# Optimization experiments

Hardware: AMD Instinct MI355X
Metric: run time of the kernel (lower is better)

The kernel has to match this reference:

```python
import jax, jax.numpy as jnp
import numpy as np

N_HEAD = 16
LN_EPS = 1e-5


def _ln(x, w, b):
    # torch LayerNorm computed in float32 then cast back (see LayerNorm.forward)
    xf = x.astype(jnp.float32)
    mu = jnp.mean(xf, axis=-1, keepdims=True)
    var = jnp.mean(jnp.square(xf - mu), axis=-1, keepdims=True)
    return ((xf - mu) * jax.lax.rsqrt(var + LN_EPS) * w + b).astype(x.dtype)


def setup_inputs() -> dict:
    key = jax.random.key(0)
    ks = jax.random.split(key, 16)
    B, S, C = 4, 1500, 1024
    A = 256  # adapter_dim
    F = 4 * C
    s = 0.02
    return {
        "x": jax.random.normal(ks[0], (B, S, C), jnp.float32),
        "Wq": jax.random.normal(ks[1], (C, C), jnp.float32) * s,
        "bq": jnp.zeros((C,), jnp.float32),
        "Wk": jax.random.normal(ks[2], (C, C), jnp.float32) * s,
        "Wv": jax.random.normal(ks[3], (C, C), jnp.float32) * s,
        "bv": jnp.zeros((C,), jnp.float32),
        "Wo": jax.random.normal(ks[4], (C, C), jnp.float32) * s,
        "bo": jnp.zeros((C,), jnp.float32),
        "ln_attn_w": jnp.ones((C,), jnp.float32),
        "ln_attn_b": jnp.zeros((C,), jnp.float32),
        "W1": jax.random.normal(ks[5], (F, C), jnp.float32) * s,
        "b1": jnp.zeros((F,), jnp.float32),
        "W2": jax.random.normal(ks[6], (C, F), jnp.float32) * s,
        "b2": jnp.zeros((C,), jnp.float32),
        "ln_mlp_w": jnp.ones((C,), jnp.float32),
        "ln_mlp_b": jnp.zeros((C,), jnp.float32),
        "Wds": jax.random.normal(ks[7], (A, C), jnp.float32) * s,
        "bds": jnp.zeros((A,), jnp.float32),
        "Wus": jax.random.normal(ks[8], (C, A), jnp.float32) * s,
        "bus": jnp.zeros((C,), jnp.float32),
    }


def reference(x, Wq, bq, Wk, Wv, bv, Wo, bo, ln_attn_w, ln_attn_b,
              W1, b1, W2, b2, ln_mlp_w, ln_mlp_b, Wds, bds, Wus, bus):
    B, S, C = x.shape
    H = N_HEAD
    D = C // H
    scale = D ** -0.25  # applied to both q and k, per qkv_attention

    # --- self-attention ---
    h = _ln(x, ln_attn_w, ln_attn_b)
    q = (h @ Wq.T + bq).reshape(B, S, H, D) * scale
    k = (h @ Wk.T).reshape(B, S, H, D) * scale  # key has no bias
    v = (h @ Wv.T + bv).reshape(B, S, H, D)
    qk = jnp.einsum("bqhd,bkhd->bhqk", q, k).astype(jnp.float32)
    w = jax.nn.softmax(qk, axis=-1).astype(x.dtype)
    wv = jnp.einsum("bhqk,bkhd->bqhd", w, v).reshape(B, S, C)
    x = x + (wv @ Wo.T + bo)

    # --- MLP (exact GELU, as nn.GELU default) ---
    h = _ln(x, ln_mlp_w, ln_mlp_b)
    x = x + (jax.nn.gelu(h @ W1.T + b1, approximate=False) @ W2.T + b2)

    # --- bottleneck adapter: x + us(gelu(ds(x))) ---
    x = x + (jax.nn.gelu(x @ Wds.T + bds, approximate=False) @ Wus.T + bus)
    return x
```

## Files before the change

### kernel.cpp

```cpp
#include <hip/hip_runtime.h>
#include <hip/hip_bf16.h>
#include <math.h>

typedef __bf16 bf16;
typedef __bf16 bf16x8 __attribute__((ext_vector_type(8)));
typedef float  f32x4  __attribute__((ext_vector_type(4)));

__device__ __forceinline__ void load16_lds(const bf16* g, bf16* l) {
    __builtin_amdgcn_global_load_lds(
        (__attribute__((address_space(1))) void*)(g),
        (__attribute__((address_space(3))) void*)(l), 16, 0, 0);
}

__device__ __forceinline__ float gelu_f(float x) {
    float u = 1.5957691216057308f * (x + 0.044715f * x * x * x);
    float e = __expf(u);
    float th = 1.0f - 2.0f / (1.0f + e);
    return 0.5f * x * (1.0f + th);
}

struct ConvArgs {
    const float* src[19];
    bf16* dst[19];
    int n[19];
    int bstart[20];
};
__global__ __launch_bounds__(256) void convert_many(ConvArgs a) {
    int blk = blockIdx.x;
    int s = 0;
    while (blk >= a.bstart[s + 1]) s++;
    const float* src = a.src[s];
    bf16* dst = a.dst[s];
    int n = a.n[s];
    int i0 = (blk - a.bstart[s]) * 2048;
#pragma unroll
    for (int e = 0; e < 8; e++) {
        int i = i0 + threadIdx.x + e * 256;
        if (i < n) dst[i] = (bf16)src[i];
    }
}

__global__ void zero_kernel(bf16* dst, int n) {
    int i = blockIdx.x * blockDim.x + threadIdx.x;
    if (i < n) dst[i] = (bf16)0.0f;
}

template<int ACT, int RES, class RT, class OT>
__global__ __launch_bounds__(256) void reduce_kernel(
    const bf16* __restrict__ P0, const bf16* __restrict__ P1,
    const bf16* __restrict__ bias, const RT* __restrict__ resid,
    OT* __restrict__ out, int nmask, int total)
{
    int i = (blockIdx.x * 256 + threadIdx.x) * 8;
    if (i >= total) return;
    bf16x8 p0 = *(const bf16x8*)(P0 + i);
    bf16x8 p1 = *(const bf16x8*)(P1 + i);
    bf16x8 bb = *(const bf16x8*)(bias + (i & nmask));
#pragma unroll
    for (int j = 0; j < 8; j++) {
        float v = (float)p0[j] + (float)p1[j] + (float)bb[j];
        if (ACT) v = gelu_f(v);
        if (RES) v += (float)resid[i + j];
        out[i + j] = (OT)v;
    }
}

template<class XT>
__global__ __launch_bounds__(256) void ln_kernel(
    const XT* __restrict__ X, const bf16* __restrict__ w,
    const bf16* __restrict__ b, bf16* __restrict__ out)
{
    const int C = 1024;
    const int row = blockIdx.x;
    const int tid = threadIdx.x;
    const XT* xr = X + (size_t)row * C;
    float x0 = (float)xr[tid * 4 + 0], x1 = (float)xr[tid * 4 + 1];
    float x2 = (float)xr[tid * 4 + 2], x3 = (float)xr[tid * 4 + 3];
    float s  = x0 + x1 + x2 + x3;
    float sq = x0*x0 + x1*x1 + x2*x2 + x3*x3;
#pragma unroll
    for (int off = 32; off >= 1; off >>= 1) {
        s  += __shfl_xor(s,  off, 64);
        sq += __shfl_xor(sq, off, 64);
    }
    __shared__ float red[8];
    int wave = tid >> 6;
    if ((tid & 63) == 0) { red[wave] = s; red[4 + wave] = sq; }
    __syncthreads();
    float ts = red[0] + red[1] + red[2] + red[3];
    float tq = red[4] + red[5] + red[6] + red[7];
    float mean = ts * (1.0f / C);
    float var  = tq * (1.0f / C) - mean * mean;
    float rstd = rsqrtf(var + 1e-5f);
    float w0 = (float)w[tid*4+0], w1 = (float)w[tid*4+1], w2 = (float)w[tid*4+2], w3 = (float)w[tid*4+3];
    float b0 = (float)b[tid*4+0], b1 = (float)b[tid*4+1], b2 = (float)b[tid*4+2], b3 = (float)b[tid*4+3];
    bf16* orow = out + (size_t)row * C + tid * 4;
    orow[0] = (bf16)((x0 - mean) * rstd * w0 + b0);
    orow[1] = (bf16)((x1 - mean) * rstd * w1 + b1);
    orow[2] = (bf16)((x2 - mean) * rstd * w2 + b2);
    orow[3] = (bf16)((x3 - mean) * rstd * w3 + b3);
}

template<int ACT, int OMODE, int BK2, class RT, class OT>
__global__ __launch_bounds__(256) void gemm_kernel(
    const bf16* __restrict__ A, const bf16* __restrict__ W,
    const bf16* __restrict__ bias, const RT* __restrict__ resid,
    OT* __restrict__ out, bf16* __restrict__ out_k, bf16* __restrict__ out_v,
    int M, int N, int K, float scale, int gmT, int gnT, int mQ, int ldK)
{
    const int lin = blockIdx.x;
    const int xcd = lin & 7;
    const int t_  = lin >> 3;
    const int mt_ = (xcd & 3) + 4 * (t_ % mQ);
    const int nt_ = (xcd >> 2) + 2 * (t_ / mQ);
    if (mt_ >= gmT || nt_ >= gnT) return;
    const int m0 = mt_ * 128;
    const int n0 = nt_ * 128;
    const int ksp = (OMODE == 3) ? blockIdx.y : 0;
    const size_t ko = (size_t)ksp * K;

    __shared__ __align__(16) bf16 As[8 * BK2 * 512];
    __shared__ __align__(16) bf16 Bs[8 * BK2 * 512];
    const int tid = threadIdx.x;
    const int wave = tid >> 6, lane = tid & 63;
    const int lane15 = lane & 15, quad = lane >> 4;
    const int wm0 = (wave >> 1) * 64;
    const int wn0 = (wave & 1) * 64;
    f32x4 acc[4][4] = {};

    int ra0 = m0 + (2 * wave)     * 16 + lane15; if (ra0 > M - 1) ra0 = M - 1;
    int ra1 = m0 + (2 * wave + 1) * 16 + lane15; if (ra1 > M - 1) ra1 = M - 1;
    const int rb0 = n0 + (2 * wave)     * 16 + lane15;
    const int rb1 = n0 + (2 * wave + 1) * 16 + lane15;
    const bf16* a0 = A + (size_t)ra0 * ldK + ko + quad * 8;
    const bf16* a1 = A + (size_t)ra1 * ldK + ko + quad * 8;
    const bf16* w0 = W + (size_t)rb0 * ldK + ko + quad * 8;
    const bf16* w1 = W + (size_t)rb1 * ldK + ko + quad * 8;

    for (int k0 = 0; k0 < K; k0 += 32 * BK2) {
#pragma unroll
        for (int kk = 0; kk < BK2; kk++) {
            load16_lds(a0 + k0 + kk * 32, &As[((2 * wave)     * BK2 + kk) * 512]);
            load16_lds(a1 + k0 + kk * 32, &As[((2 * wave + 1) * BK2 + kk) * 512]);
            load16_lds(w0 + k0 + kk * 32, &Bs[((2 * wave)     * BK2 + kk) * 512]);
            load16_lds(w1 + k0 + kk * 32, &Bs[((2 * wave + 1) * BK2 + kk) * 512]);
        }
        __syncthreads();
#pragma unroll
        for (int kk = 0; kk < BK2; kk++) {
            bf16x8 af[4], bfr[4];
#pragma unroll
            for (int tt = 0; tt < 4; tt++) {
                af[tt]  = *(const bf16x8*)(&As[(((wm0 >> 4) + tt) * BK2 + kk) * 512 + lane * 8]);
                bfr[tt] = *(const bf16x8*)(&Bs[(((wn0 >> 4) + tt) * BK2 + kk) * 512 + lane * 8]);
            }
#pragma unroll
            for (int mt = 0; mt < 4; mt++)
#pragma unroll
                for (int nt = 0; nt < 4; nt++)
                    acc[mt][nt] = __builtin_amdgcn_mfma_f32_16x16x32_bf16(
                        af[mt], bfr[nt], acc[mt][nt], 0, 0, 0);
        }
        __syncthreads();
    }

#pragma unroll
    for (int mt = 0; mt < 4; mt++) {
#pragma unroll
        for (int r = 0; r < 4; r++) {
            int gm = m0 + wm0 + mt * 16 + quad * 4 + r;
            if (gm >= M) continue;
#pragma unroll
            for (int nt = 0; nt < 4; nt++) {
                int gn = n0 + wn0 + nt * 16 + lane15;
                float v = acc[mt][nt][r];
                if (OMODE == 3) {
                    bf16* po = ksp ? out_k : (bf16*)out;
                    po[(size_t)gm * N + gn] = (bf16)v;
                    continue;
                }
                if (bias) v += (float)bias[gn];
                if (OMODE == 2) {
                    if (gn < 2048) {
                        v *= scale;
                        if (gn < 1024) v *= 1.4426950408889634f;
                    }
                } else v *= scale;
                if (ACT == 1) v = gelu_f(v);
                if (OMODE == 2) {
                    if (gn < 1024) {
                        ((bf16*)out)[(size_t)gm * 1024 + gn] = (bf16)v;
                    } else if (gn < 2048) {
                        out_k[(size_t)gm * 1024 + (gn - 1024)] = (bf16)v;
                    } else {
                        int gg = gn - 2048;
                        int bb = gm / 1500;
                        int ss = gm - bb * 1500;
                        int hh = gg >> 6, dd = gg & 63;
                        out_v[(((size_t)bb * 16 + hh) * 64 + dd) * 1536 + ss] = (bf16)v;
                    }
                } else {
                    if (resid) v += (float)resid[(size_t)gm * N + gn];
                    out[(size_t)gm * N + gn] = (OT)v;
                }
            }
        }
    }
}

__global__ __launch_bounds__(256) void flash_attn_kernel(
    const bf16* __restrict__ Q, const bf16* __restrict__ Km,
    const bf16* __restrict__ Vt, bf16* __restrict__ O)
{
    const int S = 1500, C = 1024, SP = 1536;
    const int LDP = 72;
    __shared__ __align__(16) bf16 Ks[2][8 * 512];
    __shared__ __align__(16) bf16 Vs[2][8 * 512];
    __shared__ __align__(16) bf16 Ps[4 * 16 * LDP];
    const int tid = threadIdx.x;
    const int wave = tid >> 6, lane = tid & 63;
    const int lane15 = lane & 15, quad = lane >> 4;
    const int bh = blockIdx.y;
    const int q0 = blockIdx.x * 64;
    const size_t headoff = (size_t)(bh >> 4) * S * C + (size_t)(bh & 15) * 64;
    const size_t vtoff   = (size_t)bh * 64 * SP;

    bf16x8 qf[2];
    int qr = q0 + wave * 16 + lane15; if (qr > S - 1) qr = S - 1;
    qf[0] = *(const bf16x8*)(Q + headoff + (size_t)qr * C + quad * 8);
    qf[1] = *(const bf16x8*)(Q + headoff + (size_t)qr * C + 32 + quad * 8);

    const bf16* vbase = Vt + vtoff + (size_t)(wave * 16 + lane15) * SP + quad * 8;

    auto stageKV = [&](int buf, int kt) {
        const int j0 = kt * 64;
        int kr = j0 + wave * 16 + lane15; if (kr > S - 1) kr = S - 1;
        const bf16* kbase = Km + headoff + (size_t)kr * C + quad * 8;
#pragma unroll
        for (int kk = 0; kk < 2; kk++) {
            load16_lds(kbase + kk * 32,      &Ks[buf][(wave * 2 + kk) * 512]);
            load16_lds(vbase + j0 + kk * 32, &Vs[buf][(wave * 2 + kk) * 512]);
        }
    };

    float m_run[4], l_part[4];
    f32x4 o_acc[4] = {};
#pragma unroll
    for (int r = 0; r < 4; r++) { m_run[r] = 4.0f; l_part[r] = 0.0f; }

    stageKV(0, 0);
    asm volatile("s_waitcnt vmcnt(0)" ::: "memory");
    __builtin_amdgcn_s_barrier();
    __builtin_amdgcn_sched_barrier(0);

    int cur = 0;
    for (int kt = 0; kt < 24; kt++) {
        if (kt + 1 < 24) stageKV(cur ^ 1, kt + 1);
        const int j0 = kt * 64;

        f32x4 s[4] = {};
#pragma unroll
        for (int kk = 0; kk < 2; kk++) {
#pragma unroll
            for (int nt = 0; nt < 4; nt++) {
                bf16x8 kf = *(const bf16x8*)(&Ks[cur][(nt * 2 + kk) * 512 + lane * 8]);
                s[nt] = __builtin_amdgcn_mfma_f32_16x16x32_bf16(qf[kk], kf, s[nt], 0, 0, 0);
            }
        }
        if (kt == 23) {
#pragma unroll
            for (int nt = 0; nt < 4; nt++) {
                if (j0 + nt * 16 + lane15 >= S) {
#pragma unroll
                    for (int r = 0; r < 4; r++) s[nt][r] = -1e30f;
                }
            }
        }

        float tm[4];
#pragma unroll
        for (int r = 0; r < 4; r++)
            tm[r] = fmaxf(fmaxf(s[0][r], s[1][r]), fmaxf(s[2][r], s[3][r]));
        bool rec = (tm[0] > m_run[0]) | (tm[1] > m_run[1]) |
                   (tm[2] > m_run[2]) | (tm[3] > m_run[3]);
        if (__any(rec)) {
#pragma unroll
            for (int r = 0; r < 4; r++) {
                float rm = tm[r];
#pragma unroll
                for (int off = 1; off < 16; off <<= 1) rm = fmaxf(rm, __shfl_xor(rm, off, 64));
                float mnew  = fmaxf(m_run[r], rm);
                float alpha = __builtin_amdgcn_exp2f(m_run[r] - mnew);
                m_run[r] = mnew;
                l_part[r] *= alpha;
#pragma unroll
                for (int dt = 0; dt < 4; dt++) o_acc[dt][r] *= alpha;
            }
        }

#pragma unroll
        for (int nt = 0; nt < 4; nt++) {
#pragma unroll
            for (int r = 0; r < 4; r++) {
                float p = __builtin_amdgcn_exp2f(s[nt][r] - m_run[r]);
                l_part[r] += p;
                Ps[wave * 16 * LDP + (quad * 4 + r) * LDP + nt * 16 + lane15] = (bf16)p;
            }
        }
        asm volatile("s_waitcnt lgkmcnt(0)" ::: "memory");
        __builtin_amdgcn_sched_barrier(0);
#pragma unroll
        for (int kk = 0; kk < 2; kk++) {
            bf16x8 pf = *(const bf16x8*)(&Ps[wave * 16 * LDP + lane15 * LDP + kk * 32 + quad * 8]);
#pragma unroll
            for (int dt = 0; dt < 4; dt++) {
                bf16x8 vf = *(const bf16x8*)(&Vs[cur][(dt * 2 + kk) * 512 + lane * 8]);
                o_acc[dt] = __builtin_amdgcn_mfma_f32_16x16x32_bf16(pf, vf, o_acc[dt], 0, 0, 0);
            }
        }
        if (kt + 1 < 24) {
            asm volatile("s_waitcnt vmcnt(0)" ::: "memory");
            __builtin_amdgcn_s_barrier();
            __builtin_amdgcn_sched_barrier(0);
        }
        cur ^= 1;
    }

    float l_inv[4];
#pragma unroll
    for (int r = 0; r < 4; r++) {
        float ls = l_part[r];
#pragma unroll
        for (int off = 1; off < 16; off <<= 1) ls += __shfl_xor(ls, off, 64);
        l_inv[r] = 1.0f / ls;
    }

#pragma unroll
    for (int dt = 0; dt < 4; dt++) {
#pragma unroll
        for (int r = 0; r < 4; r++) {
            int row = q0 + wave * 16 + quad * 4 + r;
            if (row < S) {
                float v = o_acc[dt][r] * l_inv[r];
                O[headoff + (size_t)row * C + dt * 16 + lane15] = (bf16)v;
            }
        }
    }
}

extern "C" void kernel_launch(void* const* d_in, const int* in_sizes, int n_in,
                              void* d_out, int out_size, void* d_ws, size_t ws_size,
                              hipStream_t stream) {
    float* out = (float*)d_out;
    const float* x_f32 = (const float*)d_in[0];
    const int M = 6000, Cc = 1024, F = 4096, Aa = 256;
    const size_t MC = (size_t)M * Cc;
    const size_t VT_ELEMS = (size_t)64 * 64 * 1536;
    bf16* ws = (bf16*)d_ws;

    bf16* h1   = ws;
    bf16* kbuf = ws + MC;
    bf16* Vt   = ws + 2 * MC;
    bf16* g    = ws + 2 * MC + VT_ELEMS;
    bf16* q    = (bf16*)d_out;
    bf16* wv   = h1;
    bf16* x1   = q;
    bf16* h2   = kbuf;
    bf16* x2   = Vt;
    bf16* aact = kbuf;
    bf16* P0o  = kbuf;
    bf16* P1o  = g;
    bf16* P0   = kbuf;
    bf16* P1   = h1;
    bf16* P0d  = h1;
    bf16* P1d  = h1 + (size_t)M * Aa;
    bf16* P0u  = g;
    bf16* P1u  = g + MC;

    size_t off = 2 * MC + VT_ELEMS + (size_t)M * F;
    bf16* Wqkv = ws + off; off += (size_t)3 * 1024 * 1024;
    bf16* bqkv = ws + off; off += 3072;
    bf16* sWo  = ws + off; off += (size_t)1024 * 1024;
    bf16* sbo  = ws + off; off += 1024;
    bf16* slnw = ws + off; off += 1024;
    bf16* slnb = ws + off; off += 1024;
    bf16* sW1  = ws + off; off += (size_t)4096 * 1024;
    bf16* sb1  = ws + off; off += 4096;
    bf16* sW2  = ws + off; off += (size_t)1024 * 4096;
    bf16* sb2  = ws + off; off += 1024;
    bf16* sln2w = ws + off; off += 1024;
    bf16* sln2b = ws + off; off += 1024;
    bf16* sWds = ws + off; off += (size_t)256 * 1024;
    bf16* sbds = ws + off; off += 256;
    bf16* sWus = ws + off; off += (size_t)1024 * 256;
    bf16* sbus = ws + off; off += 1024;

    ConvArgs ca;
    const int srcidx[19] = {1, 3, 4, 2, 5, 6, 7, 8, 9, 10, 11, 12, 13, 14, 15, 16, 17, 18, 19};
    bf16* dsts[19] = {Wqkv, Wqkv + 1048576, Wqkv + 2097152, bqkv, bqkv + 2048,
                      sWo, sbo, slnw, slnb, sW1, sb1, sW2, sb2, sln2w, sln2b,
                      sWds, sbds, sWus, sbus};
    int bacc = 0;
    for (int i = 0; i < 19; i++) {
        ca.src[i] = (const float*)d_in[srcidx[i]];
        ca.dst[i] = dsts[i];
        ca.n[i] = in_sizes[srcidx[i]];
        ca.bstart[i] = bacc;
        bacc += (ca.n[i] + 2047) / 2048;
    }
    ca.bstart[19] = bacc;

    dim3 blk(256);
    convert_many<<<bacc, blk, 0, stream>>>(ca);
    zero_kernel<<<4, blk, 0, stream>>>(bqkv + 1024, 1024);

    const float scale = 0.35355339059327373f;
    const int gmT = 47, mQ = 12;
    auto grid_for = [&](int gnT) { int nQ = (gnT + 1) >> 1; return dim3(8 * mQ * nQ); };

    ln_kernel<float><<<M, blk, 0, stream>>>(x_f32, slnw, slnb, h1);
    gemm_kernel<0, 2, 4, bf16, bf16><<<grid_for(24), blk, 0, stream>>>(
        h1, Wqkv, bqkv, (const bf16*)nullptr, q, kbuf, Vt, M, 3072, Cc, scale, gmT, 24, mQ, Cc);
    dim3 ga(24, 64);
    flash_attn_kernel<<<ga, blk, 0, stream>>>(q, kbuf, Vt, wv);

    {
        dim3 gr = grid_for(8); gr.y = 2;
        gemm_kernel<0, 3, 4, bf16, bf16><<<gr, blk, 0, stream>>>(
            wv, sWo, nullptr, (const bf16*)nullptr, P0o, P1o, nullptr,
            M, Cc, Cc / 2, 1.0f, gmT, 8, mQ, Cc);
        reduce_kernel<0, 1, float, bf16><<<(M * Cc) / 2048, blk, 0, stream>>>(
            P0o, P1o, sbo, x_f32, x1, Cc - 1, M * Cc);
    }

    ln_kernel<bf16><<<M, blk, 0, stream>>>(x1, sln2w, sln2b, h2);
    gemm_kernel<1, 0, 4, bf16, bf16><<<grid_for(32), blk, 0, stream>>>(
        h2, sW1, sb1, (const bf16*)nullptr, g, nullptr, nullptr, M, F, Cc, 1.0f, gmT, 32, mQ, Cc);

    {
        dim3 gr = grid_for(8); gr.y = 2;
        gemm_kernel<0, 3, 4, bf16, bf16><<<gr, blk, 0, stream>>>(
            g, sW2, nullptr, (const bf16*)nullptr, P0, P1, nullptr,
            M, Cc, F / 2, 1.0f, gmT, 8, mQ, F);
        reduce_kernel<0, 1, bf16, bf16><<<(M * Cc) / 2048, blk, 0, stream>>>(
            P0, P1, sb2, x1, x2, Cc - 1, M * Cc);
    }

    {
        dim3 gr = grid_for(2); gr.y = 2;
        gemm_kernel<0, 3, 4, bf16, bf16><<<gr, blk, 0, stream>>>(
            x2, sWds, nullptr, (const bf16*)nullptr, P0d, P1d, nullptr,
            M, Aa, Cc / 2, 1.0f, gmT, 2, mQ, Cc);
        reduce_kernel<1, 0, bf16, bf16><<<(M * Aa) / 2048, blk, 0, stream>>>(
            P0d, P1d, sbds, nullptr, aact, Aa - 1, M * Aa);
    }

    {
        dim3 gr = grid_for(8); gr.y = 2;
        gemm_kernel<0, 3, 4, bf16, bf16><<<gr, blk, 0, stream>>>(
            aact, sWus, nullptr, (const bf16*)nullptr, P0u, P1u, nullptr,
            M, Cc, Aa / 2, 1.0f, gmT, 8, mQ, Aa);
        reduce_kernel<0, 1, bf16, float><<<(M * Cc) / 2048, blk, 0, stream>>>(
            P0u, P1u, sbus, x2, out, Cc - 1, M * Cc);
    }
}
```

Measured before the change: 750.6 us.

## Fuse out-proj reduce with LayerNorm, add 256-row GEMM for MLP up-projection, shrink K-step

Merges the out-projection split-K reduction with the second LayerNorm into one row kernel, removing a full round trip of x1 through memory and one launch. Adds a 512-thread GEMM with 256x128 tiles for the W1 up-projection, so each W1 tile loaded into LDS is reused across twice as many rows. Hardcodes the generic GEMM K-step to 64 instead of 128, which shrinks LDS use and may raise occupancy but doubles the number of barrier iterations. The wide kernel's larger tile reduces the block count and could hurt load balance.

Measured after the change: 690.4 us. -8.0%, faster.

```diff
diff --git a/kernel.cpp b/kernel.cpp
--- a/kernel.cpp
+++ b/kernel.cpp
@@ -62,6 +62,51 @@
         if (ACT) v = gelu_f(v);
         if (RES) v += (float)resid[i + j];
         out[i + j] = (OT)v;
+    }
+}
+
+__global__ __launch_bounds__(256) void reduce_ln_kernel(
+    const bf16* __restrict__ P0, const bf16* __restrict__ P1,
+    const bf16* __restrict__ bo, const float* __restrict__ xres,
+    bf16* __restrict__ x1, const bf16* __restrict__ w,
+    const bf16* __restrict__ b, bf16* __restrict__ h2)
+{
+    const int C = 1024;
+    const int row = blockIdx.x;
+    const int tid = threadIdx.x;
+    const size_t base = (size_t)row * C + tid * 4;
+    float v[4];
+#pragma unroll
+    for (int j = 0; j < 4; j++) {
+        v[j] = (float)P0[base + j] + (float)P1[base + j]
+             + (float)bo[tid * 4 + j] + xres[base + j];
+    }
+    bf16* xo = x1 + base;
+#pragma unroll
+    for (int j = 0; j < 4; j++) xo[j] = (bf16)v[j];
+    float q0 = (float)xo[0], q1 = (float)xo[1], q2 = (float)xo[2], q3 = (float)xo[3];
+    float s  = q0 + q1 + q2 + q3;
+    float sq = q0*q0 + q1*q1 + q2*q2 + q3*q3;
+#pragma unroll
+    for (int off = 32; off >= 1; off >>= 1) {
+        s  += __shfl_xor(s,  off, 64);
+        sq += __shfl_xor(sq, off, 64);
+    }
+    __shared__ float red[8];
+    int wave = tid >> 6;
+    if ((tid & 63) == 0) { red[wave] = s; red[4 + wave] = sq; }
+    __syncthreads();
+    float ts = red[0] + red[1] + red[2] + red[3];
+    float tq = red[4] + red[5] + red[6] + red[7];
+    float mean = ts * (1.0f / C);
+    float var  = tq * (1.0f / C) - mean * mean;
+    float rstd = rsqrtf(var + 1e-5f);
+    bf16* orow = h2 + base;
+#pragma unroll
+    for (int j = 0; j < 4; j++) {
+        float wj = (float)w[tid * 4 + j], bj = (float)b[tid * 4 + j];
+        float qj = (j == 0 ? q0 : j == 1 ? q1 : j == 2 ? q2 : q3);
+        orow[j] = (bf16)((qj - mean) * rstd * wj + bj);
     }
 }
 
@@ -101,7 +146,7 @@
     orow[3] = (bf16)((x3 - mean) * rstd * w3 + b3);
 }
 
-template<int ACT, int OMODE, int BK2, class RT, class OT>
+template<int ACT, int OMODE, class RT, class OT>
 __global__ __launch_bounds__(256) void gemm_kernel(
     const bf16* __restrict__ A, const bf16* __restrict__ W,
     const bf16* __restrict__ bias, const RT* __restrict__ resid,
@@ -119,8 +164,8 @@
     const int ksp = (OMODE == 3) ? blockIdx.y : 0;
     const size_t ko = (size_t)ksp * K;
 
-    __shared__ __align__(16) bf16 As[8 * BK2 * 512];
-    __shared__ __align__(16) bf16 Bs[8 * BK2 * 512];
+    __shared__ __align__(16) bf16 As[16 * 512];
+    __shared__ __align__(16) bf16 Bs[16 * 512];
     const int tid = threadIdx.x;
     const int wave = tid >> 6, lane = tid & 63;
     const int lane15 = lane & 15, quad = lane >> 4;
@@ -137,22 +182,22 @@
     const bf16* w0 = W + (size_t)rb0 * ldK + ko + quad * 8;
     const bf16* w1 = W + (size_t)rb1 * ldK + ko + quad * 8;
 
-    for (int k0 = 0; k0 < K; k0 += 32 * BK2) {
-#pragma unroll
-        for (int kk = 0; kk < BK2; kk++) {
-            load16_lds(a0 + k0 + kk * 32, &As[((2 * wave)     * BK2 + kk) * 512]);
-            load16_lds(a1 + k0 + kk * 32, &As[((2 * wave + 1) * BK2 + kk) * 512]);
-            load16_lds(w0 + k0 + kk * 32, &Bs[((2 * wave)     * BK2 + kk) * 512]);
-            load16_lds(w1 + k0 + kk * 32, &Bs[((2 * wave + 1) * BK2 + kk) * 512]);
+    for (int k0 = 0; k0 < K; k0 += 64) {
+#pragma unroll
+        for (int kk = 0; kk < 2; kk++) {
+            load16_lds(a0 + k0 + kk * 32, &As[((2 * wave)     * 2 + kk) * 512]);
+            load16_lds(a1 + k0 + kk * 32, &As[((2 * wave + 1) * 2 + kk) * 512]);
+            load16_lds(w0 + k0 + kk * 32, &Bs[((2 * wave)     * 2 + kk) * 512]);
+            load16_lds(w1 + k0 + kk * 32, &Bs[((2 * wave + 1) * 2 + kk) * 512]);
         }
         __syncthreads();
 #pragma unroll
-        for (int kk = 0; kk < BK2; kk++) {
+        for (int kk = 0; kk < 2; kk++) {
             bf16x8 af[4], bfr[4];
 #pragma unroll
             for (int tt = 0; tt < 4; tt++) {
-                af[tt]  = *(const bf16x8*)(&As[(((wm0 >> 4) + tt) * BK2 + kk) * 512 + lane * 8]);
-                bfr[tt] = *(const bf16x8*)(&Bs[(((wn0 >> 4) + tt) * BK2 + kk) * 512 + lane * 8]);
+                af[tt]  = *(const bf16x8*)(&As[(((wm0 >> 4) + tt) * 2 + kk) * 512 + lane * 8]);
+                bfr[tt] = *(const bf16x8*)(&Bs[(((wn0 >> 4) + tt) * 2 + kk) * 512 + lane * 8]);
             }
 #pragma unroll
             for (int mt = 0; mt < 4; mt++)
@@ -208,6 +253,80 @@
     }
 }
 
+template<int ACT, class OT>
+__global__ __launch_bounds__(512) void gemm_wide_kernel(
+    const bf16* __restrict__ A, const bf16* __restrict__ W,
+    const bf16* __restrict__ bias, OT* __restrict__ out,
+    int M, int N, int K, int gmT, int gnT, int mQ, int ldK)
+{
+    const int lin = blockIdx.x;
+    const int xcd = lin & 7;
+    const int t_  = lin >> 3;
+    const int mt_ = (xcd & 3) + 4 * (t_ % mQ);
+    const int nt_ = (xcd >> 2) + 2 * (t_ / mQ);
+    if (mt_ >= gmT || nt_ >= gnT) return;
+    const int m0 = mt_ * 256;
+    const int n0 = nt_ * 128;
+
+    __shared__ __align__(16) bf16 As[32 * 512];
+    __shared__ __align__(16) bf16 Bs[16 * 512];
+    const int tid = threadIdx.x;
+    const int wave = tid >> 6, lane = tid & 63;
+    const int lane15 = lane & 15, quad = lane >> 4;
+    const int wm0 = (wave >> 1) * 64;
+    const int wn0 = (wave & 1) * 64;
+    f32x4 acc[4][4] = {};
+
+    int ra0 = m0 + (2 * wave)     * 16 + lane15; if (ra0 > M - 1) ra0 = M - 1;
+    int ra1 = m0 + (2 * wave + 1) * 16 + lane15; if (ra1 > M - 1) ra1 = M - 1;
+    const int rb = n0 + wave * 16 + lane15;
+    const bf16* a0 = A + (size_t)ra0 * ldK + quad * 8;
+    const bf16* a1 = A + (size_t)ra1 * ldK + quad * 8;
+    const bf16* w0 = W + (size_t)rb * ldK + quad * 8;
+
+    for (int k0 = 0; k0 < K; k0 += 64) {
+#pragma unroll
+        for (int kk = 0; kk < 2; kk++) {
+            load16_lds(a0 + k0 + kk * 32, &As[((2 * wave)     * 2 + kk) * 512]);
+            load16_lds(a1 + k0 + kk * 32, &As[((2 * wave + 1) * 2 + kk) * 512]);
+            load16_lds(w0 + k0 + kk * 32, &Bs[(wave * 2 + kk) * 512]);
+        }
+        __syncthreads();
+#pragma unroll
+        for (int kk = 0; kk < 2; kk++) {
+            bf16x8 af[4], bfr[4];
+#pragma unroll
+            for (int tt = 0; tt < 4; tt++) {
+                af[tt]  = *(const bf16x8*)(&As[(((wm0 >> 4) + tt) * 2 + kk) * 512 + lane * 8]);
+                bfr[tt] = *(const bf16x8*)(&Bs[(((wn0 >> 4) + tt) * 2 + kk) * 512 + lane * 8]);
+            }
+#pragma unroll
+            for (int mt = 0; mt < 4; mt++)
+#pragma unroll
+                for (int nt = 0; nt < 4; nt++)
+                    acc[mt][nt] = __builtin_amdgcn_mfma_f32_16x16x32_bf16(
+                        af[mt], bfr[nt], acc[mt][nt], 0, 0, 0);
+        }
+        __syncthreads();
+    }
+
+#pragma unroll
+    for (int mt = 0; mt < 4; mt++) {
+#pragma unroll
+        for (int r = 0; r < 4; r++) {
+            int gm = m0 + wm0 + mt * 16 + quad * 4 + r;
+            if (gm >= M) continue;
+#pragma unroll
+            for (int nt = 0; nt < 4; nt++) {
+                int gn = n0 + wn0 + nt * 16 + lane15;
+                float v = acc[mt][nt][r] + (float)bias[gn];
+                if (ACT == 1) v = gelu_f(v);
+                out[(size_t)gm * N + gn] = (OT)v;
+            }
+        }
+    }
+}
+
 __global__ __launch_bounds__(256) void flash_attn_kernel(
     const bf16* __restrict__ Q, const bf16* __restrict__ Km,
     const bf16* __restrict__ Vt, bf16* __restrict__ O)
@@ -411,35 +530,37 @@
     ca.bstart[19] = bacc;
 
     dim3 blk(256);
+    dim3 blk512(512);
     convert_many<<<bacc, blk, 0, stream>>>(ca);
     zero_kernel<<<4, blk, 0, stream>>>(bqkv + 1024, 1024);
 
     const float scale = 0.35355339059327373f;
     const int gmT = 47, mQ = 12;
     auto grid_for = [&](int gnT) { int nQ = (gnT + 1) >> 1; return dim3(8 * mQ * nQ); };
+    const int gmTw = 24, mQw = 6;
+    auto gridw_for = [&](int gnT) { int nQ = (gnT + 1) >> 1; return dim3(8 * mQw * nQ); };
 
     ln_kernel<float><<<M, blk, 0, stream>>>(x_f32, slnw, slnb, h1);
-    gemm_kernel<0, 2, 4, bf16, bf16><<<grid_for(24), blk, 0, stream>>>(
+    gemm_kernel<0, 2, bf16, bf16><<<grid_for(24), blk, 0, stream>>>(
         h1, Wqkv, bqkv, (const bf16*)nullptr, q, kbuf, Vt, M, 3072, Cc, scale, gmT, 24, mQ, Cc);
     dim3 ga(24, 64);
     flash_attn_kernel<<<ga, blk, 0, stream>>>(q, kbuf, Vt, wv);
 
     {
         dim3 gr = grid_for(8); gr.y = 2;
-        gemm_kernel<0, 3, 4, bf16, bf16><<<gr, blk, 0, stream>>>(
+        gemm_kernel<0, 3, bf16, bf16><<<gr, blk, 0, stream>>>(
             wv, sWo, nullptr, (const bf16*)nullptr, P0o, P1o, nullptr,
             M, Cc, Cc / 2, 1.0f, gmT, 8, mQ, Cc);
-        reduce_kernel<0, 1, float, bf16><<<(M * Cc) / 2048, blk, 0, stream>>>(
-            P0o, P1o, sbo, x_f32, x1, Cc - 1, M * Cc);
-    }
-
-    ln_kernel<bf16><<<M, blk, 0, stream>>>(x1, sln2w, sln2b, h2);
-    gemm_kernel<1, 0, 4, bf16, bf16><<<grid_for(32), blk, 0, stream>>>(
-        h2, sW1, sb1, (const bf16*)nullptr, g, nullptr, nullptr, M, F, Cc, 1.0f, gmT, 32, mQ, Cc);
+        reduce_ln_kernel<<<M, blk, 0, stream>>>(
+            P0o, P1o, sbo, x_f32, x1, sln2w, sln2b, h2);
+    }
+
+    gemm_wide_kernel<1, bf16><<<gridw_for(32), blk512, 0, stream>>>(
+        h2, sW1, sb1, g, M, F, Cc, gmTw, 32, mQw, Cc);
 
     {
         dim3 gr = grid_for(8); gr.y = 2;
-        gemm_kernel<0, 3, 4, bf16, bf16><<<gr, blk, 0, stream>>>(
+        gemm_kernel<0, 3, bf16, bf16><<<gr, blk, 0, stream>>>(
             g, sW2, nullptr, (const bf16*)nullptr, P0, P1, nullptr,
             M, Cc, F / 2, 1.0f, gmT, 8, mQ, F);
         reduce_kernel<0, 1, bf16, bf16><<<(M * Cc) / 2048, blk, 0, stream>>>(
@@ -448,7 +569,7 @@
 
     {
         dim3 gr = grid_for(2); gr.y = 2;
-        gemm_kernel<0, 3, 4, bf16, bf16><<<gr, blk, 0, stream>>>(
+        gemm_kernel<0, 3, bf16, bf16><<<gr, blk, 0, stream>>>(
             x2, sWds, nullptr, (const bf16*)nullptr, P0d, P1d, nullptr,
             M, Aa, Cc / 2, 1.0f, gmT, 2, mQ, Cc);
         reduce_kernel<1, 0, bf16, bf16><<<(M * Aa) / 2048, blk, 0, stream>>>(
@@ -457,7 +578,7 @@
 
     {
         dim3 gr = grid_for(8); gr.y = 2;
-        gemm_kernel<0, 3, 4, bf16, bf16><<<gr, blk, 0, stream>>>(
+        gemm_kernel<0, 3, bf16, bf16><<<gr, blk, 0, stream>>>(
             aact, sWus, nullptr, (const bf16*)nullptr, P0u, P1u, nullptr,
             M, Cc, Aa / 2, 1.0f, gmT, 8, mQ, Aa);
         reduce_kernel<0, 1, bf16, float><<<(M * Cc) / 2048, blk, 0, stream>>>(
```
